# Optimization experiments

Hardware: AMD Instinct MI355X
Metric: run time of the kernel (lower is better)

The kernel has to match this reference:

```python
import jax, jax.numpy as jnp
import numpy as np

N_NODES = 50000
N_EDGES = 1_250_000
D = 64
EPS = 1e-5


def gcn_conv(x, src, dst, W, b, n_nodes):
    # PyG GCNConv: h = x @ W; add self loops; sym-normalized scatter-add; + bias
    h = x @ W  # [N, D_out]
    loop = jnp.arange(n_nodes, dtype=src.dtype)
    s = jnp.concatenate([src, loop])
    d = jnp.concatenate([dst, loop])
    deg = jax.ops.segment_sum(jnp.ones_like(d, dtype=h.dtype), d, num_segments=n_nodes)
    dinv = jax.lax.rsqrt(deg)  # deg >= 1 due to self loops
    norm = dinv[s] * dinv[d]  # [E+N]
    msg = h[s] * norm[:, None]  # gather + per-edge scale
    out = jax.ops.segment_sum(msg, d, num_segments=n_nodes)
    return out + b


def prelu(x, a):
    return jnp.where(x >= 0, x, a * x)


def layer_norm_node(x, gamma, beta):
    mu = jnp.mean(x, axis=-1, keepdims=True)
    var = jnp.mean(jnp.square(x - mu), axis=-1, keepdims=True)
    return (x - mu) * jax.lax.rsqrt(var + EPS) * gamma + beta


def setup_inputs() -> dict:
    key = jax.random.key(0)
    ks = jax.random.split(key, 10)
    X = jax.random.normal(ks[0], (N_NODES, D), dtype=jnp.float32)
    edge_index = jax.random.randint(ks[1], (2, N_EDGES), 0, N_NODES, dtype=jnp.int32)
    scale = 1.0 / np.sqrt(D)
    W1 = jax.random.normal(ks[2], (D, D), dtype=jnp.float32) * scale
    b1 = jnp.zeros((D,), dtype=jnp.float32)
    W2 = jax.random.normal(ks[3], (D, D), dtype=jnp.float32) * scale
    b2 = jnp.zeros((D,), dtype=jnp.float32)
    W3 = jax.random.normal(ks[4], (D, D), dtype=jnp.float32) * scale
    b3 = jnp.zeros((D,), dtype=jnp.float32)
    prelu_a = jnp.asarray(0.25, dtype=jnp.float32)  # single shared PReLU param
    ln_gamma = jnp.ones((D,), dtype=jnp.float32)
    ln_beta = jnp.zeros((D,), dtype=jnp.float32)
    return {"X": X, "W1": W1, "b1": b1, "W2": W2, "b2": b2, "W3": W3,
            "b3": b3, "prelu_a": prelu_a, "ln_gamma": ln_gamma,
            "ln_beta": ln_beta, "edge_index": edge_index}


def reference(X, W1, b1, W2, b2, W3, b3, prelu_a, ln_gamma, ln_beta, edge_index):
    src, dst = edge_index[0], edge_index[1]
    n = X.shape[0]
    h = gcn_conv(X, src, dst, W1, b1, n)
    h = prelu(h, prelu_a)
    h = gcn_conv(h, src, dst, W2, b2, n)
    h = prelu(h, prelu_a)
    h = gcn_conv(h, src, dst, W3, b3, n)
    return layer_norm_node(h, ln_gamma, ln_beta)
```

## Files before the change

### kernel.cpp

```cpp
#include <hip/hip_runtime.h>

#define D 64
#define BK_SHIFT 6
#define TCAP 4096
#define CSTRIDE 6144
#define NBLK_M 512
#define MCH 2560

__device__ __forceinline__ float bfbits2f(unsigned short b) {
    union { unsigned int u; float f; } c;
    c.u = ((unsigned int)b) << 16;
    return c.f;
}

__device__ __forceinline__ unsigned short f2bfbits(float f) {
    union { float f; unsigned int u; } c;
    c.f = f;
    unsigned int u = c.u;
    unsigned int lsb = (u >> 16) & 1u;
    u += 0x7fffu + lsb;
    return (unsigned short)(u >> 16);
}

__device__ __forceinline__ float ldmix(const void* p, size_t i, int isf32) {
    return isf32 ? ((const float*)p)[i] : bfbits2f(((const unsigned short*)p)[i]);
}

__device__ __forceinline__ float rlane(float v, int l) {
    return __int_as_float(__builtin_amdgcn_readlane(__float_as_int(v), l));
}

#define OW1 0
#define OW2 4096
#define OW3 8192
#define OB1 12288
#define OB2 12352
#define OB3 12416
#define OG  12480
#define OBE 12544
#define OPA 12608

__global__ void cvt_params_kernel(const void* W1, const void* b1, const void* W2, const void* b2,
                                  const void* W3, const void* b3, const void* pa, const void* g,
                                  const void* be, int* __restrict__ flag,
                                  float* __restrict__ P) {
    __shared__ int sbad;
    int t = threadIdx.x;
    if (t == 0) sbad = 0;
    __syncthreads();
    {
        float v = bfbits2f(((const unsigned short*)W1)[t]);
        if (!(v == v) || fabsf(v) > 1e4f) atomicOr(&sbad, 1);
    }
    __syncthreads();
    int isf = sbad ? 1 : 0;
    if (t == 0) *flag = isf;
    for (int i = t; i < D * D; i += 256) {
        P[OW1 + i] = ldmix(W1, i, isf);
        P[OW2 + i] = ldmix(W2, i, isf);
        P[OW3 + i] = ldmix(W3, i, isf);
    }
    if (t < D) {
        P[OB1 + t] = ldmix(b1, t, isf);
        P[OB2 + t] = ldmix(b2, t, isf);
        P[OB3 + t] = ldmix(b3, t, isf);
        P[OG  + t] = ldmix(g,  t, isf);
        P[OBE + t] = ldmix(be, t, isf);
    }
    if (t == 0) P[OPA] = ldmix(pa, 0, isf);
}

__global__ void __launch_bounds__(256)
binAm_kernel(const int* __restrict__ src, const int* __restrict__ dst,
             int E, int NB, int CH, int* __restrict__ gcur,
             unsigned int* __restrict__ tmp) {
    __shared__ int ls[MCH];
    __shared__ int ld[MCH];
    __shared__ int h[1024];
    int t = threadIdx.x, bb = blockIdx.x;
    int beg = bb * CH, end = beg + CH; if (end > E) end = E;
    int m = end - beg;
    bool staged = (m <= MCH);
    for (int i = t; i < NB; i += 256) h[i] = 0;
    __syncthreads();
    for (int i = t; i < m; i += 256) {
        int d = dst[beg + i];
        if (staged) { ld[i] = d; ls[i] = src[beg + i]; }
        atomicAdd(&h[d >> BK_SHIFT], 1);
    }
    __syncthreads();
    for (int b = t; b < NB; b += 256) {
        int c = h[b];
        h[b] = c ? atomicAdd(&gcur[b], c) : 0;
    }
    __syncthreads();
    for (int i = t; i < m; i += 256) {
        int d = staged ? ld[i] : dst[beg + i];
        int s = staged ? ls[i] : src[beg + i];
        int bk = d >> BK_SHIFT;
        int p = atomicAdd(&h[bk], 1);
        if (p < TCAP)
            tmp[(size_t)bk * TCAP + p] = ((unsigned int)s << BK_SHIFT) | (unsigned int)(d & 63);
    }
}

__global__ void binB_kernel(const unsigned int* __restrict__ tmp, const int* __restrict__ gcur,
                            int* __restrict__ row_beg, int* __restrict__ cnt,
                            float* __restrict__ dinv, int* __restrict__ col,
                            const void* __restrict__ X, const int* __restrict__ flag,
                            unsigned short* __restrict__ Xs, int N) {
    __shared__ unsigned int ent[TCAP];
    __shared__ int lv[64], lpv[64], lpe[64], lcur[64];
    __shared__ float ldv[64];
    int b = blockIdx.x, t = threadIdx.x;
    int beg = b * TCAP;
    int colbase = b * CSTRIDE;
    int m = gcur[b]; if (m > TCAP) m = TCAP;
    if (t < 64) lv[t] = 0;
    __syncthreads();
    for (int i = t; i < m; i += 256) {
        unsigned int e = tmp[beg + i];
        ent[i] = e;
        atomicAdd(&lv[e & 63u], 1);
    }
    __syncthreads();
    if (t < 64) {
        int v  = lv[t];
        int pv = (v + 31) & ~31;
        if (pv == 0) pv = 32;
        int incl = pv;
#pragma unroll
        for (int off = 1; off < 64; off <<= 1) {
            int u = __shfl_up(incl, off, 64);
            if (t >= off) incl += u;
        }
        int pexcl = incl - pv;
        lpv[t]  = pv;
        lpe[t]  = pexcl;
        lcur[t] = pexcl;
        float dv = rsqrtf((float)(v + 1));
        ldv[t] = dv;
        int node = b * 64 + t;
        if (node < N) {
            row_beg[node] = colbase + pexcl;
            cnt[node]     = pv;
            dinv[node]    = dv;
        }
    }
    __syncthreads();
    for (int i = t; i < m; i += 256) {
        unsigned int e = ent[i];
        int p = atomicAdd(&lcur[e & 63u], 1);
        col[colbase + p] = (int)(e >> BK_SHIFT);
    }
    for (int i = t; i < 64 * 32; i += 256) {
        int nl = i >> 5, j = i & 31;
        int idx = lv[nl] + j;
        if (idx < lpv[nl]) col[colbase + lpe[nl] + idx] = N;
    }
    int isf = *flag;
    for (int i = t; i < 64 * 64; i += 256) {
        int nl = i >> 6, f = i & 63;
        int node = b * 64 + nl;
        if (node < N)
            Xs[(size_t)node * D + f] = f2bfbits(ldv[nl] * ldmix(X, (size_t)node * D + f, isf));
    }
}


__device__ __forceinline__ void acc8(float* a, uint4 v) {
    a[0] += bfbits2f((unsigned short)(v.x & 0xffffu));
    a[1] += bfbits2f((unsigned short)(v.x >> 16));
    a[2] += bfbits2f((unsigned short)(v.y & 0xffffu));
    a[3] += bfbits2f((unsigned short)(v.y >> 16));
    a[4] += bfbits2f((unsigned short)(v.z & 0xffffu));
    a[5] += bfbits2f((unsigned short)(v.z >> 16));
    a[6] += bfbits2f((unsigned short)(v.w & 0xffffu));
    a[7] += bfbits2f((unsigned short)(v.w >> 16));
}

__device__ __forceinline__ void agg_tail(const unsigned short* __restrict__ Xs,
                                         const int* __restrict__ col, int beg, int pc,
                                         int slot, int sub, float (&x)[8]) {
    for (int c = 32; c < pc; c += 32) {
        int4 s = *(const int4*)(col + beg + c + 4 * slot);
        uint4 v0 = *((const uint4*)(Xs + ((size_t)s.x << 6)) + sub);
        uint4 v1 = *((const uint4*)(Xs + ((size_t)s.y << 6)) + sub);
        uint4 v2 = *((const uint4*)(Xs + ((size_t)s.z << 6)) + sub);
        uint4 v3 = *((const uint4*)(Xs + ((size_t)s.w << 6)) + sub);
        acc8(x, v0); acc8(x, v1); acc8(x, v2); acc8(x, v3);
    }
}

__device__ __forceinline__ void quad_main(const unsigned short* __restrict__ Xs,
        const int* __restrict__ row_beg, const int* __restrict__ cnt,
        const int* __restrict__ col, const float* __restrict__ dinv,
        const float* __restrict__ Wt, int base, int n, int lane,
        float& dn0, float& dn1, float& dn2, float& dn3,
        float& a0, float& a1, float& a2, float& a3)
{
    const int slot = lane >> 3, sub = lane & 7;
    bool v1 = (base + 1) < n, v2 = (base + 2) < n, v3 = (base + 3) < n;
    int i0 = base, i1 = v1 ? base + 1 : n, i2 = v2 ? base + 2 : n, i3 = v3 ? base + 3 : n;
    int beg0 = row_beg[base];
    int beg1 = v1 ? row_beg[base + 1] : beg0;
    int beg2 = v2 ? row_beg[base + 2] : beg0;
    int beg3 = v3 ? row_beg[base + 3] : beg0;
    int pc0 = cnt[base];
    int pc1 = v1 ? cnt[base + 1] : 32;
    int pc2 = v2 ? cnt[base + 2] : 32;
    int pc3 = v3 ? cnt[base + 3] : 32;
    dn0 = dinv[base];
    dn1 = v1 ? dinv[base + 1] : 0.f;
    dn2 = v2 ? dinv[base + 2] : 0.f;
    dn3 = v3 ? dinv[base + 3] : 0.f;

    uint4 sv0 = *((const uint4*)(Xs + ((size_t)i0 << 6)) + sub);
    uint4 sv1 = *((const uint4*)(Xs + ((size_t)i1 << 6)) + sub);
    uint4 sv2 = *((const uint4*)(Xs + ((size_t)i2 << 6)) + sub);
    uint4 sv3 = *((const uint4*)(Xs + ((size_t)i3 << 6)) + sub);
    int4 c0 = *(const int4*)(col + beg0 + 4 * slot);
    int4 c1 = *(const int4*)(col + beg1 + 4 * slot);
    int4 c2 = *(const int4*)(col + beg2 + 4 * slot);
    int4 c3 = *(const int4*)(col + beg3 + 4 * slot);
    uint4 r00 = *((const uint4*)(Xs + ((size_t)c0.x << 6)) + sub);
    uint4 r01 = *((const uint4*)(Xs + ((size_t)c0.y << 6)) + sub);
    uint4 r02 = *((const uint4*)(Xs + ((size_t)c0.z << 6)) + sub);
    uint4 r03 = *((const uint4*)(Xs + ((size_t)c0.w << 6)) + sub);
    uint4 r10 = *((const uint4*)(Xs + ((size_t)c1.x << 6)) + sub);
    uint4 r11 = *((const uint4*)(Xs + ((size_t)c1.y << 6)) + sub);
    uint4 r12 = *((const uint4*)(Xs + ((size_t)c1.z << 6)) + sub);
    uint4 r13 = *((const uint4*)(Xs + ((size_t)c1.w << 6)) + sub);
    uint4 r20 = *((const uint4*)(Xs + ((size_t)c2.x << 6)) + sub);
    uint4 r21 = *((const uint4*)(Xs + ((size_t)c2.y << 6)) + sub);
    uint4 r22 = *((const uint4*)(Xs + ((size_t)c2.z << 6)) + sub);
    uint4 r23 = *((const uint4*)(Xs + ((size_t)c2.w << 6)) + sub);
    uint4 r30 = *((const uint4*)(Xs + ((size_t)c3.x << 6)) + sub);
    uint4 r31 = *((const uint4*)(Xs + ((size_t)c3.y << 6)) + sub);
    uint4 r32 = *((const uint4*)(Xs + ((size_t)c3.z << 6)) + sub);
    uint4 r33 = *((const uint4*)(Xs + ((size_t)c3.w << 6)) + sub);

    float x0[8], x1[8], x2[8], x3[8];
#pragma unroll
    for (int j = 0; j < 8; ++j) { x0[j] = 0.f; x1[j] = 0.f; x2[j] = 0.f; x3[j] = 0.f; }
    acc8(x0, r00); acc8(x0, r01); acc8(x0, r02); acc8(x0, r03);
    acc8(x1, r10); acc8(x1, r11); acc8(x1, r12); acc8(x1, r13);
    acc8(x2, r20); acc8(x2, r21); acc8(x2, r22); acc8(x2, r23);
    acc8(x3, r30); acc8(x3, r31); acc8(x3, r32); acc8(x3, r33);
    agg_tail(Xs, col, beg0, pc0, slot, sub, x0);
    agg_tail(Xs, col, beg1, pc1, slot, sub, x1);
    agg_tail(Xs, col, beg2, pc2, slot, sub, x2);
    agg_tail(Xs, col, beg3, pc3, slot, sub, x3);
#pragma unroll
    for (int off = 8; off < 64; off <<= 1) {
#pragma unroll
        for (int j = 0; j < 8; ++j) {
            x0[j] += __shfl_xor(x0[j], off, 64);
            x1[j] += __shfl_xor(x1[j], off, 64);
            x2[j] += __shfl_xor(x2[j], off, 64);
            x3[j] += __shfl_xor(x3[j], off, 64);
        }
    }
    acc8(x0, sv0); acc8(x1, sv1); acc8(x2, sv2); acc8(x3, sv3);

    a0 = 0.f; a1 = 0.f; a2 = 0.f; a3 = 0.f;
    const float* wt = Wt + lane * 68;
#pragma unroll
    for (int kc = 0; kc < 8; ++kc) {
        float4 wa = *(const float4*)(wt + kc * 8);
        float4 wb = *(const float4*)(wt + kc * 8 + 4);
#define GQ(j, wv) { float w_ = (wv); \
        a0 = fmaf(rlane(x0[j], kc), w_, a0); \
        a1 = fmaf(rlane(x1[j], kc), w_, a1); \
        a2 = fmaf(rlane(x2[j], kc), w_, a2); \
        a3 = fmaf(rlane(x3[j], kc), w_, a3); }
        GQ(0, wa.x) GQ(1, wa.y) GQ(2, wa.z) GQ(3, wa.w)
        GQ(4, wb.x) GQ(5, wb.y) GQ(6, wb.z) GQ(7, wb.w)
#undef GQ
    }
}

__global__ void __launch_bounds__(256)
agg_gemm_kernel(const unsigned short* __restrict__ Xs,
                const int* __restrict__ row_beg, const int* __restrict__ cnt,
                const int* __restrict__ col, const float* __restrict__ dinv,
                const float* __restrict__ W, const float* __restrict__ b,
                const float* __restrict__ pa,
                unsigned short* __restrict__ Xout, int n) {
    __shared__ float Wt[64 * 68];
    int t = threadIdx.x;
    for (int i = t; i < D * D; i += 256) Wt[(i & 63) * 68 + (i >> 6)] = W[i];
    __syncthreads();
    int wid = t >> 6, lane = t & 63;
    int base = blockIdx.x * 16 + wid * 4;
    if (base >= n) return;
    float bl = b[lane];
    float pr = pa[0];
    float dn0, dn1, dn2, dn3, a0, a1, a2, a3;
    quad_main(Xs, row_beg, cnt, col, dinv, Wt, base, n, lane,
              dn0, dn1, dn2, dn3, a0, a1, a2, a3);
    a0 = fmaf(dn0, a0, bl); a1 = fmaf(dn1, a1, bl);
    a2 = fmaf(dn2, a2, bl); a3 = fmaf(dn3, a3, bl);
    a0 = (a0 >= 0.f) ? a0 : pr * a0;
    a1 = (a1 >= 0.f) ? a1 : pr * a1;
    a2 = (a2 >= 0.f) ? a2 : pr * a2;
    a3 = (a3 >= 0.f) ? a3 : pr * a3;
    a0 *= dn0; a1 *= dn1; a2 *= dn2; a3 *= dn3;
    Xout[(size_t)base * D + lane] = f2bfbits(a0);
    if (base + 1 < n) Xout[(size_t)(base + 1) * D + lane] = f2bfbits(a1);
    if (base + 2 < n) Xout[(size_t)(base + 2) * D + lane] = f2bfbits(a2);
    if (base + 3 < n) Xout[(size_t)(base + 3) * D + lane] = f2bfbits(a3);
}

__global__ void __launch_bounds__(256)
agg_gemm_ln_kernel(const unsigned short* __restrict__ Xs,
                   const int* __restrict__ row_beg, const int* __restrict__ cnt,
                   const int* __restrict__ col, const float* __restrict__ dinv,
                   const float* __restrict__ W, const float* __restrict__ b,
                   const float* __restrict__ g, const float* __restrict__ be,
                   const int* __restrict__ flag, void* __restrict__ out, int n) {
    __shared__ float Wt[64 * 68];
    int t = threadIdx.x;
    for (int i = t; i < D * D; i += 256) Wt[(i & 63) * 68 + (i >> 6)] = W[i];
    __syncthreads();
    int wid = t >> 6, lane = t & 63;
    int base = blockIdx.x * 16 + wid * 4;
    if (base >= n) return;
    int   isf = *flag;
    float bl  = b[lane];
    float gl  = g[lane];
    float bel = be[lane];
    float dn0, dn1, dn2, dn3, a0, a1, a2, a3;
    quad_main(Xs, row_beg, cnt, col, dinv, Wt, base, n, lane,
              dn0, dn1, dn2, dn3, a0, a1, a2, a3);
    a0 = fmaf(dn0, a0, bl); a1 = fmaf(dn1, a1, bl);
    a2 = fmaf(dn2, a2, bl); a3 = fmaf(dn3, a3, bl);
    float s0 = a0, s1 = a1, s2 = a2, s3 = a3;
#pragma unroll
    for (int off = 32; off > 0; off >>= 1) {
        s0 += __shfl_xor(s0, off, 64); s1 += __shfl_xor(s1, off, 64);
        s2 += __shfl_xor(s2, off, 64); s3 += __shfl_xor(s3, off, 64);
    }
    float mu0 = s0 * (1.f / 64.f), mu1 = s1 * (1.f / 64.f);
    float mu2 = s2 * (1.f / 64.f), mu3 = s3 * (1.f / 64.f);
    float d0 = a0 - mu0, d1 = a1 - mu1, d2 = a2 - mu2, d3 = a3 - mu3;
    float q0 = d0 * d0, q1 = d1 * d1, q2 = d2 * d2, q3 = d3 * d3;
#pragma unroll
    for (int off = 32; off > 0; off >>= 1) {
        q0 += __shfl_xor(q0, off, 64); q1 += __shfl_xor(q1, off, 64);
        q2 += __shfl_xor(q2, off, 64); q3 += __shfl_xor(q3, off, 64);
    }
    float r0 = rsqrtf(q0 * (1.f / 64.f) + 1e-5f);
    float r1 = rsqrtf(q1 * (1.f / 64.f) + 1e-5f);
    float r2 = rsqrtf(q2 * (1.f / 64.f) + 1e-5f);
    float r3 = rsqrtf(q3 * (1.f / 64.f) + 1e-5f);
    float o0 = d0 * r0 * gl + bel;
    float o1 = d1 * r1 * gl + bel;
    float o2 = d2 * r2 * gl + bel;
    float o3 = d3 * r3 * gl + bel;
    size_t oi = (size_t)base * D + lane;
    if (isf) {
        ((float*)out)[oi] = o0;
        if (base + 1 < n) ((float*)out)[oi + 64]  = o1;
        if (base + 2 < n) ((float*)out)[oi + 128] = o2;
        if (base + 3 < n) ((float*)out)[oi + 192] = o3;
    } else {
        ((unsigned short*)out)[oi] = f2bfbits(o0);
        if (base + 1 < n) ((unsigned short*)out)[oi + 64]  = f2bfbits(o1);
        if (base + 2 < n) ((unsigned short*)out)[oi + 128] = f2bfbits(o2);
        if (base + 3 < n) ((unsigned short*)out)[oi + 192] = f2bfbits(o3);
    }
}


extern "C" void kernel_launch(void* const* d_in, const int* in_sizes, int n_in,
                              void* d_out, int out_size, void* d_ws, size_t ws_size,
                              hipStream_t stream) {
    const void* X   = d_in[0];
    const void* W1  = d_in[1];
    const void* b1  = d_in[2];
    const void* W2  = d_in[3];
    const void* b2  = d_in[4];
    const void* W3  = d_in[5];
    const void* b3  = d_in[6];
    const void* pa  = d_in[7];
    const void* g   = d_in[8];
    const void* be  = d_in[9];
    const int*  ei  = (const int*)d_in[10];

    int N = in_sizes[0] / D;
    int E = in_sizes[10] / 2;
    int NB = (N + 63) >> BK_SHIFT;
    int CH = (E + NBLK_M - 1) / NBLK_M;
    const int* src = ei;
    const int* dst = ei + E;

    char* p = (char*)d_ws;
    auto alloc = [&](size_t bytes) { void* q = (void*)p; p += (bytes + 255) & ~(size_t)255; return q; };
    int*            flag       = (int*)alloc(4);
    int*            gcur       = (int*)alloc((size_t)NB * 4);
    int*            row_beg    = (int*)alloc((size_t)N * 4);
    int*            cnt        = (int*)alloc((size_t)N * 4);
    float*          dinv       = (float*)alloc((size_t)N * 4);
    int*            col        = (int*)alloc((size_t)NB * CSTRIDE * 4);
    unsigned int*   tmp        = (unsigned int*)alloc((size_t)NB * TCAP * 4);
    float*          P          = (float*)alloc((size_t)(OPA + 1) * 4);
    unsigned short* Xs         = (unsigned short*)alloc((size_t)(N + 1) * D * 2);
    unsigned short* Xs2        = (unsigned short*)alloc((size_t)(N + 1) * D * 2);
    (void)ws_size; (void)n_in; (void)out_size;

    (void)hipMemsetAsync(gcur, 0, (size_t)NB * 4, stream);
    (void)hipMemsetAsync(Xs  + (size_t)N * D, 0, D * 2, stream);
    (void)hipMemsetAsync(Xs2 + (size_t)N * D, 0, D * 2, stream);

    cvt_params_kernel<<<1, 256, 0, stream>>>(W1, b1, W2, b2, W3, b3, pa, g, be, flag, P);

    binAm_kernel<<<NBLK_M, 256, 0, stream>>>(src, dst, E, NB, CH, gcur, tmp);
    binB_kernel<<<NB, 256, 0, stream>>>(tmp, gcur, row_beg, cnt, dinv, col, X, flag, Xs, N);

    int ngb = (N + 15) / 16;

    agg_gemm_kernel   <<<ngb, 256, 0, stream>>>(Xs,  row_beg, cnt, col, dinv, P + OW1, P + OB1, P + OPA, Xs2, N);
    agg_gemm_kernel   <<<ngb, 256, 0, stream>>>(Xs2, row_beg, cnt, col, dinv, P + OW2, P + OB2, P + OPA, Xs,  N);
    agg_gemm_ln_kernel<<<ngb, 256, 0, stream>>>(Xs,  row_beg, cnt, col, dinv, P + OW3, P + OB3, P + OG, P + OBE, flag, d_out, N);
}
```

Before: 272.1 us.

## Split bf16 feature rows into two 32-wide planes and aggregate each in separate passes

```diff
diff --git a/kernel.cpp b/kernel.cpp
--- a/kernel.cpp
+++ b/kernel.cpp
@@ -108,7 +108,8 @@
                             int* __restrict__ row_beg, int* __restrict__ cnt,
                             float* __restrict__ dinv, int* __restrict__ col,
                             const void* __restrict__ X, const int* __restrict__ flag,
-                            unsigned short* __restrict__ Xs, int N) {
+                            unsigned short* __restrict__ XsL, unsigned short* __restrict__ XsH,
+                            int N) {
     __shared__ unsigned int ent[TCAP];
     __shared__ int lv[64], lpv[64], lpe[64], lcur[64];
     __shared__ float ldv[64];
@@ -162,8 +163,11 @@
     for (int i = t; i < 64 * 64; i += 256) {
         int nl = i >> 6, f = i & 63;
         int node = b * 64 + nl;
-        if (node < N)
-            Xs[(size_t)node * D + f] = f2bfbits(ldv[nl] * ldmix(X, (size_t)node * D + f, isf));
+        if (node < N) {
+            unsigned short v = f2bfbits(ldv[nl] * ldmix(X, (size_t)node * D + f, isf));
+            if (f < 32) XsL[(size_t)node * 32 + f] = v;
+            else        XsH[(size_t)node * 32 + (f - 32)] = v;
+        }
     }
 }
 
@@ -179,27 +183,24 @@
     a[7] += bfbits2f((unsigned short)(v.w >> 16));
 }
 
-__device__ __forceinline__ void agg_tail(const unsigned short* __restrict__ Xs,
-                                         const int* __restrict__ col, int beg, int pc,
-                                         int slot, int sub, float (&x)[8]) {
+__device__ __forceinline__ void plane_tail(const unsigned short* __restrict__ Xp,
+                                           const int* __restrict__ col, int beg, int pc,
+                                           int slot, int sub, float (&x)[8]) {
     for (int c = 32; c < pc; c += 32) {
-        int4 s = *(const int4*)(col + beg + c + 4 * slot);
-        uint4 v0 = *((const uint4*)(Xs + ((size_t)s.x << 6)) + sub);
-        uint4 v1 = *((const uint4*)(Xs + ((size_t)s.y << 6)) + sub);
-        uint4 v2 = *((const uint4*)(Xs + ((size_t)s.z << 6)) + sub);
-        uint4 v3 = *((const uint4*)(Xs + ((size_t)s.w << 6)) + sub);
-        acc8(x, v0); acc8(x, v1); acc8(x, v2); acc8(x, v3);
-    }
-}
-
-__device__ __forceinline__ void quad_main(const unsigned short* __restrict__ Xs,
+        int2 s = *(const int2*)(col + beg + c + 2 * slot);
+        uint4 va = ((const uint4*)(Xp + ((size_t)s.x << 5)))[sub];
+        uint4 vb = ((const uint4*)(Xp + ((size_t)s.y << 5)))[sub];
+        acc8(x, va); acc8(x, vb);
+    }
+}
+
+__device__ __forceinline__ void quad_plane_main(const unsigned short* __restrict__ Xp,
         const int* __restrict__ row_beg, const int* __restrict__ cnt,
-        const int* __restrict__ col, const float* __restrict__ dinv,
-        const float* __restrict__ Wt, int base, int n, int lane,
-        float& dn0, float& dn1, float& dn2, float& dn3,
+        const int* __restrict__ col, const float* __restrict__ Wt, int khalf,
+        int base, int n, int lane,
         float& a0, float& a1, float& a2, float& a3)
 {
-    const int slot = lane >> 3, sub = lane & 7;
+    const int slot = lane >> 2, sub = lane & 3;
     bool v1 = (base + 1) < n, v2 = (base + 2) < n, v3 = (base + 3) < n;
     int i0 = base, i1 = v1 ? base + 1 : n, i2 = v2 ? base + 2 : n, i3 = v3 ? base + 3 : n;
     int beg0 = row_beg[base];
@@ -210,49 +211,37 @@
     int pc1 = v1 ? cnt[base + 1] : 32;
     int pc2 = v2 ? cnt[base + 2] : 32;
     int pc3 = v3 ? cnt[base + 3] : 32;
-    dn0 = dinv[base];
-    dn1 = v1 ? dinv[base + 1] : 0.f;
-    dn2 = v2 ? dinv[base + 2] : 0.f;
-    dn3 = v3 ? dinv[base + 3] : 0.f;
-
-    uint4 sv0 = *((const uint4*)(Xs + ((size_t)i0 << 6)) + sub);
-    uint4 sv1 = *((const uint4*)(Xs + ((size_t)i1 << 6)) + sub);
-    uint4 sv2 = *((const uint4*)(Xs + ((size_t)i2 << 6)) + sub);
-    uint4 sv3 = *((const uint4*)(Xs + ((size_t)i3 << 6)) + sub);
-    int4 c0 = *(const int4*)(col + beg0 + 4 * slot);
-    int4 c1 = *(const int4*)(col + beg1 + 4 * slot);
-    int4 c2 = *(const int4*)(col + beg2 + 4 * slot);
-    int4 c3 = *(const int4*)(col + beg3 + 4 * slot);
-    uint4 r00 = *((const uint4*)(Xs + ((size_t)c0.x << 6)) + sub);
-    uint4 r01 = *((const uint4*)(Xs + ((size_t)c0.y << 6)) + sub);
-    uint4 r02 = *((const uint4*)(Xs + ((size_t)c0.z << 6)) + sub);
-    uint4 r03 = *((const uint4*)(Xs + ((size_t)c0.w << 6)) + sub);
-    uint4 r10 = *((const uint4*)(Xs + ((size_t)c1.x << 6)) + sub);
-    uint4 r11 = *((const uint4*)(Xs + ((size_t)c1.y << 6)) + sub);
-    uint4 r12 = *((const uint4*)(Xs + ((size_t)c1.z << 6)) + sub);
-    uint4 r13 = *((const uint4*)(Xs + ((size_t)c1.w << 6)) + sub);
-    uint4 r20 = *((const uint4*)(Xs + ((size_t)c2.x << 6)) + sub);
-    uint4 r21 = *((const uint4*)(Xs + ((size_t)c2.y << 6)) + sub);
-    uint4 r22 = *((const uint4*)(Xs + ((size_t)c2.z << 6)) + sub);
-    uint4 r23 = *((const uint4*)(Xs + ((size_t)c2.w << 6)) + sub);
-    uint4 r30 = *((const uint4*)(Xs + ((size_t)c3.x << 6)) + sub);
-    uint4 r31 = *((const uint4*)(Xs + ((size_t)c3.y << 6)) + sub);
-    uint4 r32 = *((const uint4*)(Xs + ((size_t)c3.z << 6)) + sub);
-    uint4 r33 = *((const uint4*)(Xs + ((size_t)c3.w << 6)) + sub);
+
+    uint4 sv0 = ((const uint4*)(Xp + ((size_t)i0 << 5)))[sub];
+    uint4 sv1 = ((const uint4*)(Xp + ((size_t)i1 << 5)))[sub];
+    uint4 sv2 = ((const uint4*)(Xp + ((size_t)i2 << 5)))[sub];
+    uint4 sv3 = ((const uint4*)(Xp + ((size_t)i3 << 5)))[sub];
+    int2 c0 = *(const int2*)(col + beg0 + 2 * slot);
+    int2 c1 = *(const int2*)(col + beg1 + 2 * slot);
+    int2 c2 = *(const int2*)(col + beg2 + 2 * slot);
+    int2 c3 = *(const int2*)(col + beg3 + 2 * slot);
+    uint4 r0a = ((const uint4*)(Xp + ((size_t)c0.x << 5)))[sub];
+    uint4 r0b = ((const uint4*)(Xp + ((size_t)c0.y << 5)))[sub];
+    uint4 r1a = ((const uint4*)(Xp + ((size_t)c1.x << 5)))[sub];
+    uint4 r1b = ((const uint4*)(Xp + ((size_t)c1.y << 5)))[sub];
+    uint4 r2a = ((const uint4*)(Xp + ((size_t)c2.x << 5)))[sub];
+    uint4 r2b = ((const uint4*)(Xp + ((size_t)c2.y << 5)))[sub];
+    uint4 r3a = ((const uint4*)(Xp + ((size_t)c3.x << 5)))[sub];
+    uint4 r3b = ((const uint4*)(Xp + ((size_t)c3.y << 5)))[sub];
 
     float x0[8], x1[8], x2[8], x3[8];
 #pragma unroll
     for (int j = 0; j < 8; ++j) { x0[j] = 0.f; x1[j] = 0.f; x2[j] = 0.f; x3[j] = 0.f; }
-    acc8(x0, r00); acc8(x0, r01); acc8(x0, r02); acc8(x0, r03);
-    acc8(x1, r10); acc8(x1, r11); acc8(x1, r12); acc8(x1, r13);
-    acc8(x2, r20); acc8(x2, r21); acc8(x2, r22); acc8(x2, r23);
-    acc8(x3, r30); acc8(x3, r31); acc8(x3, r32); acc8(x3, r33);
-    agg_tail(Xs, col, beg0, pc0, slot, sub, x0);
-    agg_tail(Xs, col, beg1, pc1, slot, sub, x1);
-    agg_tail(Xs, col, beg2, pc2, slot, sub, x2);
-    agg_tail(Xs, col, beg3, pc3, slot, sub, x3);
-#pragma unroll
-    for (int off = 8; off < 64; off <<= 1) {
+    acc8(x0, r0a); acc8(x0, r0b);
+    acc8(x1, r1a); acc8(x1, r1b);
+    acc8(x2, r2a); acc8(x2, r2b);
+    acc8(x3, r3a); acc8(x3, r3b);
+    plane_tail(Xp, col, beg0, pc0, slot, sub, x0);
+    plane_tail(Xp, col, beg1, pc1, slot, sub, x1);
+    plane_tail(Xp, col, beg2, pc2, slot, sub, x2);
+    plane_tail(Xp, col, beg3, pc3, slot, sub, x3);
+#pragma unroll
+    for (int off = 4; off < 64; off <<= 1) {
 #pragma unroll
         for (int j = 0; j < 8; ++j) {
             x0[j] += __shfl_xor(x0[j], off, 64);
@@ -264,16 +253,16 @@
     acc8(x0, sv0); acc8(x1, sv1); acc8(x2, sv2); acc8(x3, sv3);
 
     a0 = 0.f; a1 = 0.f; a2 = 0.f; a3 = 0.f;
-    const float* wt = Wt + lane * 68;
-#pragma unroll
-    for (int kc = 0; kc < 8; ++kc) {
-        float4 wa = *(const float4*)(wt + kc * 8);
-        float4 wb = *(const float4*)(wt + kc * 8 + 4);
-#define GQ(j, wv) { float w_ = (wv); \
-        a0 = fmaf(rlane(x0[j], kc), w_, a0); \
-        a1 = fmaf(rlane(x1[j], kc), w_, a1); \
-        a2 = fmaf(rlane(x2[j], kc), w_, a2); \
-        a3 = fmaf(rlane(x3[j], kc), w_, a3); }
+    const float* wt = Wt + lane * 68 + khalf;
+#pragma unroll
+    for (int s = 0; s < 4; ++s) {
+        float4 wa = *(const float4*)(wt + s * 8);
+        float4 wb = *(const float4*)(wt + s * 8 + 4);
+#define GQ(j, wv) { float wq_ = (wv); \
+        a0 = fmaf(rlane(x0[j], s), wq_, a0); \
+        a1 = fmaf(rlane(x1[j], s), wq_, a1); \
+        a2 = fmaf(rlane(x2[j], s), wq_, a2); \
+        a3 = fmaf(rlane(x3[j], s), wq_, a3); }
         GQ(0, wa.x) GQ(1, wa.y) GQ(2, wa.z) GQ(3, wa.w)
         GQ(4, wb.x) GQ(5, wb.y) GQ(6, wb.z) GQ(7, wb.w)
 #undef GQ
@@ -281,12 +270,10 @@
 }
 
 __global__ void __launch_bounds__(256)
-agg_gemm_kernel(const unsigned short* __restrict__ Xs,
-                const int* __restrict__ row_beg, const int* __restrict__ cnt,
-                const int* __restrict__ col, const float* __restrict__ dinv,
-                const float* __restrict__ W, const float* __restrict__ b,
-                const float* __restrict__ pa,
-                unsigned short* __restrict__ Xout, int n) {
+aggA_kernel(const unsigned short* __restrict__ XpL,
+            const int* __restrict__ row_beg, const int* __restrict__ cnt,
+            const int* __restrict__ col, const float* __restrict__ W,
+            float* __restrict__ po, int n) {
     __shared__ float Wt[64 * 68];
     int t = threadIdx.x;
     for (int i = t; i < D * D; i += 256) Wt[(i & 63) * 68 + (i >> 6)] = W[i];
@@ -294,11 +281,43 @@
     int wid = t >> 6, lane = t & 63;
     int base = blockIdx.x * 16 + wid * 4;
     if (base >= n) return;
+    float a0, a1, a2, a3;
+    quad_plane_main(XpL, row_beg, cnt, col, Wt, 0, base, n, lane, a0, a1, a2, a3);
+    size_t pb = (size_t)base * 64 + lane;
+    po[pb] = a0;
+    if (base + 1 < n) po[pb + 64]  = a1;
+    if (base + 2 < n) po[pb + 128] = a2;
+    if (base + 3 < n) po[pb + 192] = a3;
+}
+
+__global__ void __launch_bounds__(256)
+aggB_kernel(const unsigned short* __restrict__ XpH,
+            const int* __restrict__ row_beg, const int* __restrict__ cnt,
+            const int* __restrict__ col, const float* __restrict__ dinv,
+            const float* __restrict__ W, const float* __restrict__ b,
+            const float* __restrict__ pa, const float* __restrict__ po,
+            unsigned short* __restrict__ YL, unsigned short* __restrict__ YH, int n) {
+    __shared__ float Wt[64 * 68];
+    int t = threadIdx.x;
+    for (int i = t; i < D * D; i += 256) Wt[(i & 63) * 68 + (i >> 6)] = W[i];
+    __syncthreads();
+    int wid = t >> 6, lane = t & 63;
+    int base = blockIdx.x * 16 + wid * 4;
+    if (base >= n) return;
+    bool v1 = (base + 1) < n, v2 = (base + 2) < n, v3 = (base + 3) < n;
+    float dn0 = dinv[base];
+    float dn1 = v1 ? dinv[base + 1] : 0.f;
+    float dn2 = v2 ? dinv[base + 2] : 0.f;
+    float dn3 = v3 ? dinv[base + 3] : 0.f;
     float bl = b[lane];
     float pr = pa[0];
-    float dn0, dn1, dn2, dn3, a0, a1, a2, a3;
-    quad_main(Xs, row_beg, cnt, col, dinv, Wt, base, n, lane,
-              dn0, dn1, dn2, dn3, a0, a1, a2, a3);
+    float a0, a1, a2, a3;
+    quad_plane_main(XpH, row_beg, cnt, col, Wt, 32, base, n, lane, a0, a1, a2, a3);
+    size_t pb = (size_t)base * 64 + lane;
+    a0 += po[pb];
+    if (v1) a1 += po[pb + 64];
+    if (v2) a2 += po[pb + 128];
+    if (v3) a3 += po[pb + 192];
     a0 = fmaf(dn0, a0, bl); a1 = fmaf(dn1, a1, bl);
     a2 = fmaf(dn2, a2, bl); a3 = fmaf(dn3, a3, bl);
     a0 = (a0 >= 0.f) ? a0 : pr * a0;
@@ -306,19 +325,23 @@
     a2 = (a2 >= 0.f) ? a2 : pr * a2;
     a3 = (a3 >= 0.f) ? a3 : pr * a3;
     a0 *= dn0; a1 *= dn1; a2 *= dn2; a3 *= dn3;
-    Xout[(size_t)base * D + lane] = f2bfbits(a0);
-    if (base + 1 < n) Xout[(size_t)(base + 1) * D + lane] = f2bfbits(a1);
-    if (base + 2 < n) Xout[(size_t)(base + 2) * D + lane] = f2bfbits(a2);
-    if (base + 3 < n) Xout[(size_t)(base + 3) * D + lane] = f2bfbits(a3);
+    int lo = lane < 32;
+    size_t si = (size_t)base * 32 + (lane & 31);
+    unsigned short* Y0 = lo ? YL : YH;
+    Y0[si] = f2bfbits(a0);
+    if (v1) (lo ? YL : YH)[si + 32]  = f2bfbits(a1);
+    if (v2) (lo ? YL : YH)[si + 64]  = f2bfbits(a2);
+    if (v3) (lo ? YL : YH)[si + 96]  = f2bfbits(a3);
 }
 
 __global__ void __launch_bounds__(256)
-agg_gemm_ln_kernel(const unsigned short* __restrict__ Xs,
-                   const int* __restrict__ row_beg, const int* __restrict__ cnt,
-                   const int* __restrict__ col, const float* __restrict__ dinv,
-                   const float* __restrict__ W, const float* __restrict__ b,
-                   const float* __restrict__ g, const float* __restrict__ be,
-                   const int* __restrict__ flag, void* __restrict__ out, int n) {
+aggB_ln_kernel(const unsigned short* __restrict__ XpH,
+               const int* __restrict__ row_beg, const int* __restrict__ cnt,
+               const int* __restrict__ col, const float* __restrict__ dinv,
+               const float* __restrict__ W, const float* __restrict__ b,
+               const float* __restrict__ g, const float* __restrict__ be,
+               const int* __restrict__ flag, const float* __restrict__ po,
+               void* __restrict__ out, int n) {
     __shared__ float Wt[64 * 68];
     int t = threadIdx.x;
     for (int i = t; i < D * D; i += 256) Wt[(i & 63) * 68 + (i >> 6)] = W[i];
@@ -326,13 +349,22 @@
     int wid = t >> 6, lane = t & 63;
     int base = blockIdx.x * 16 + wid * 4;
     if (base >= n) return;
+    bool v1 = (base + 1) < n, v2 = (base + 2) < n, v3 = (base + 3) < n;
+    float dn0 = dinv[base];
+    float dn1 = v1 ? dinv[base + 1] : 0.f;
+    float dn2 = v2 ? dinv[base + 2] : 0.f;
+    float dn3 = v3 ? dinv[base + 3] : 0.f;
     int   isf = *flag;
     float bl  = b[lane];
     float gl  = g[lane];
     float bel = be[lane];
-    float dn0, dn1, dn2, dn3, a0, a1, a2, a3;
-    quad_main(Xs, row_beg, cnt, col, dinv, Wt, base, n, lane,
-              dn0, dn1, dn2, dn3, a0, a1, a2, a3);
+    float a0, a1, a2, a3;
+    quad_plane_main(XpH, row_beg, cnt, col, Wt, 32, base, n, lane, a0, a1, a2, a3);
+    size_t pb = (size_t)base * 64 + lane;
+    a0 += po[pb];
+    if (v1) a1 += po[pb + 64];
+    if (v2) a2 += po[pb + 128];
+    if (v3) a3 += po[pb + 192];
     a0 = fmaf(dn0, a0, bl); a1 = fmaf(dn1, a1, bl);
     a2 = fmaf(dn2, a2, bl); a3 = fmaf(dn3, a3, bl);
     float s0 = a0, s1 = a1, s2 = a2, s3 = a3;
@@ -361,14 +393,14 @@
     size_t oi = (size_t)base * D + lane;
     if (isf) {
         ((float*)out)[oi] = o0;
-        if (base + 1 < n) ((float*)out)[oi + 64]  = o1;
-        if (base + 2 < n) ((float*)out)[oi + 128] = o2;
-        if (base + 3 < n) ((float*)out)[oi + 192] = o3;
+        if (v1) ((float*)out)[oi + 64]  = o1;
+        if (v2) ((float*)out)[oi + 128] = o2;
+        if (v3) ((float*)out)[oi + 192] = o3;
     } else {
         ((unsigned short*)out)[oi] = f2bfbits(o0);
-        if (base + 1 < n) ((unsigned short*)out)[oi + 64]  = f2bfbits(o1);
-        if (base + 2 < n) ((unsigned short*)out)[oi + 128] = f2bfbits(o2);
-        if (base + 3 < n) ((unsigned short*)out)[oi + 192] = f2bfbits(o3);
+        if (v1) ((unsigned short*)out)[oi + 64]  = f2bfbits(o1);
+        if (v2) ((unsigned short*)out)[oi + 128] = f2bfbits(o2);
+        if (v3) ((unsigned short*)out)[oi + 192] = f2bfbits(o3);
     }
 }
 
@@ -405,22 +437,30 @@
     int*            col        = (int*)alloc((size_t)NB * CSTRIDE * 4);
     unsigned int*   tmp        = (unsigned int*)alloc((size_t)NB * TCAP * 4);
     float*          P          = (float*)alloc((size_t)(OPA + 1) * 4);
-    unsigned short* Xs         = (unsigned short*)alloc((size_t)(N + 1) * D * 2);
-    unsigned short* Xs2        = (unsigned short*)alloc((size_t)(N + 1) * D * 2);
+    float*          po         = (float*)alloc((size_t)N * 64 * 4);
+    unsigned short* XsL        = (unsigned short*)alloc((size_t)(N + 1) * 32 * 2);
+    unsigned short* XsH        = (unsigned short*)alloc((size_t)(N + 1) * 32 * 2);
+    unsigned short* YsL        = (unsigned short*)alloc((size_t)(N + 1) * 32 * 2);
+    unsigned short* YsH        = (unsigned short*)alloc((size_t)(N + 1) * 32 * 2);
     (void)ws_size; (void)n_in; (void)out_size;
 
     (void)hipMemsetAsync(gcur, 0, (size_t)NB * 4, stream);
-    (void)hipMemsetAsync(Xs  + (size_t)N * D, 0, D * 2, stream);
-    (void)hipMemsetAsync(Xs2 + (size_t)N * D, 0, D * 2, stream);
+    (void)hipMemsetAsync(XsL + (size_t)N * 32, 0, 64, stream);
+    (void)hipMemsetAsync(XsH + (size_t)N * 32, 0, 64, stream);
+    (void)hipMemsetAsync(YsL + (size_t)N * 32, 0, 64, stream);
+    (void)hipMemsetAsync(YsH + (size_t)N * 32, 0, 64, stream);
 
     cvt_params_kernel<<<1, 256, 0, stream>>>(W1, b1, W2, b2, W3, b3, pa, g, be, flag, P);
 
     binAm_kernel<<<NBLK_M, 256, 0, stream>>>(src, dst, E, NB, CH, gcur, tmp);
-    binB_kernel<<<NB, 256, 0, stream>>>(tmp, gcur, row_beg, cnt, dinv, col, X, flag, Xs, N);
+    binB_kernel<<<NB, 256, 0, stream>>>(tmp, gcur, row_beg, cnt, dinv, col, X, flag, XsL, XsH, N);
 
     int ngb = (N + 15) / 16;
 
-    agg_gemm_kernel   <<<ngb, 256, 0, stream>>>(Xs,  row_beg, cnt, col, dinv, P + OW1, P + OB1, P + OPA, Xs2, N);
-    agg_gemm_kernel   <<<ngb, 256, 0, stream>>>(Xs2, row_beg, cnt, col, dinv, P + OW2, P + OB2, P + OPA, Xs,  N);
-    agg_gemm_ln_kernel<<<ngb, 256, 0, stream>>>(Xs,  row_beg, cnt, col, dinv, P + OW3, P + OB3, P + OG, P + OBE, flag, d_out, N);
-}
+    aggA_kernel<<<ngb, 256, 0, stream>>>(XsL, row_beg, cnt, col, P + OW1, po, N);
+    aggB_kernel<<<ngb, 256, 0, stream>>>(XsH, row_beg, cnt, col, dinv, P + OW1, P + OB1, P + OPA, po, YsL, YsH, N);
+    aggA_kernel<<<ngb, 256, 0, stream>>>(YsL, row_beg, cnt, col, P + OW2, po, N);
+    aggB_kernel<<<ngb, 256, 0, stream>>>(YsH, row_beg, cnt, col, dinv, P + OW2, P + OB2, P + OPA, po, XsL, XsH, N);
+    aggA_kernel<<<ngb, 256, 0, stream>>>(XsL, row_beg, cnt, col, P + OW3, po, N);
+    aggB_ln_kernel<<<ngb, 256, 0, stream>>>(XsH, row_beg, cnt, col, dinv, P + OW3, P + OB3, P + OG, P + OBE, flag, po, d_out, N);
+}
```

After: 336.2 us. 1.24x slower.
